# Performance work log

Hardware: AMD Instinct MI355X
Metric: run time of the kernel (lower is better)

Reference implementation:

```python
import jax, jax.numpy as jnp
import numpy as np

TEMP = 0.5
K_SEL = 20
NEG_SLOPE = 0.1


def setup_inputs() -> dict:
    key = jax.random.key(0)
    ks = jax.random.split(key, 12)
    B, N = 64, 20000
    F1, F2, D = 512, 256, 128
    init = lambda k, shape, fan: (jax.random.normal(k, shape) / np.sqrt(fan)).astype(jnp.float32)
    return {
        "patient_embedding": jax.random.normal(ks[0], (B, F1), dtype=jnp.float32),
        "gene_embedding": jax.random.normal(ks[1], (N, F2), dtype=jnp.float32),
        "Wq": init(ks[2], (F1, D), F1), "bq": jnp.zeros((D,), jnp.float32),
        "Wk": init(ks[3], (F2, D), F2), "bk": jnp.zeros((D,), jnp.float32),
        "Wv": init(ks[4], (F2, D), F2), "bv": jnp.zeros((D,), jnp.float32),
        "W1": init(ks[5], (2 * D, D), 2 * D), "b1": jnp.zeros((D,), jnp.float32),
        "w2": init(ks[6], (D,), D), "b2": jnp.zeros((), jnp.float32),
    }


def reference(patient_embedding, gene_embedding, Wq, bq, Wk, bk, Wv, bv, W1, b1, w2, b2):
    B = patient_embedding.shape[0]
    N = gene_embedding.shape[0]
    D = Wq.shape[1]

    Q = patient_embedding @ Wq + bq          # [B, D]
    Km = gene_embedding @ Wk + bk            # [N, D]
    V = gene_embedding @ Wv + bv             # [N, D]

    # MLP attention on cat([Q_exp, K_exp]); split W1 to avoid materializing [B,N,2D]
    q_part = Q @ W1[:D]                      # [B, D]
    k_part = Km @ W1[D:]                     # [N, D]
    h = jax.nn.leaky_relu(q_part[:, None, :] + k_part[None, :, :] + b1, NEG_SLOPE)  # [B, N, D]
    sim = h @ w2 + b2                        # [B, N]
    logits = sim / TEMP

    # gumbel-softmax, hard=True, independent noise per (b, k) row
    g = jax.random.gumbel(jax.random.key(42), (B, K_SEL, N), dtype=logits.dtype)
    y_soft = jax.nn.softmax((logits[:, None, :] + g) / TEMP, axis=-1)   # [B, K, N]
    y_hard = jax.nn.one_hot(jnp.argmax(y_soft, axis=-1), N, dtype=y_soft.dtype)
    masks = y_hard - jax.lax.stop_gradient(y_soft) + y_soft             # straight-through

    topk_values = jnp.einsum("bkn,nd->bkd", masks, V)                   # [B, K, D]
    scores = jnp.einsum("bd,bkd->bk", Q, topk_values) / np.sqrt(D).astype(np.float32)
    weights = jax.nn.softmax(scores, axis=-1)                           # [B, K] (dropout = eval/identity)
    context = jnp.einsum("bk,bkd->bd", weights, topk_values)            # [B, D]
    return context
```

## Files before the change

kernel.cpp:

```cpp
#include <hip/hip_runtime.h>

#define NG 20000

__device__ __forceinline__ unsigned rotl32(unsigned x, int r) {
  return __builtin_amdgcn_alignbit(x, x, 32 - r);
}

__device__ __forceinline__ void threefry2x32(unsigned x0, unsigned x1,
                                             unsigned& o0, unsigned& o1) {
  const unsigned ks0 = 0u;
  const unsigned ks1 = 42u;
  const unsigned ks2 = 0x1BD11BDAu ^ 0u ^ 42u;
  x0 += ks0; x1 += ks1;
#define TFR(r) { x0 += x1; x1 = rotl32(x1, (r)); x1 ^= x0; }
  TFR(13) TFR(15) TFR(26) TFR(6)
  x0 += ks1; x1 += ks2 + 1u;
  TFR(17) TFR(29) TFR(16) TFR(24)
  x0 += ks2; x1 += ks0 + 2u;
  TFR(13) TFR(15) TFR(26) TFR(6)
  x0 += ks0; x1 += ks1 + 3u;
  TFR(17) TFR(29) TFR(16) TFR(24)
  x0 += ks1; x1 += ks2 + 4u;
  TFR(13) TFR(15) TFR(26) TFR(6)
  x0 += ks2; x1 += ks0 + 5u;
#undef TFR
  o0 = x0; o1 = x1;
}

__device__ __forceinline__ unsigned tfbits(unsigned ctr) {
  unsigned o0, o1;
  threefry2x32(0u, ctr, o0, o1);
  return o0 ^ o1;
}

__device__ __forceinline__ float gumbel32(unsigned bits) {
  float f = __uint_as_float((bits >> 9) | 0x3f800000u) - 1.0f;
  float u = fmaxf(f, 1.17549435e-38f);
  const float l2u = __log2f(u);
  return fmaf(-0.69314718056f, __log2f(-l2u), 0.3665129206f);
}

__device__ __forceinline__ double gumbel64(unsigned bits) {
  float f = __uint_as_float((bits >> 9) | 0x3f800000u) - 1.0f;
  double u = (double)fmaxf(f, 1.17549435e-38f);
  return -log(-log(u));
}

__device__ __forceinline__ unsigned long long packcell(double v, int n) {
  unsigned long long u = (unsigned long long)__double_as_longlong(v);
  u = (u >> 63) ? ~u : (u | 0x8000000000000000ull);
  return (u & 0xFFFFFFFFFFFF8000ull) | (unsigned long long)(32767 - n);
}

__device__ __forceinline__ unsigned long long packscreen(float v, int n) {
  unsigned u = __float_as_uint(v);
  u = (u >> 31) ? ~u : (u | 0x80000000u);
  return ((unsigned long long)u << 32) | (unsigned)n;
}

__global__ __launch_bounds__(128) void kprep(
    const float* __restrict__ pe, const float* __restrict__ Wq,
    const float* __restrict__ bq, const float* __restrict__ Wk,
    const float* __restrict__ bk, const float* __restrict__ W1,
    const float* __restrict__ b1, const float* __restrict__ w2,
    float* __restrict__ Wf32, double* __restrict__ qbT,
    float* __restrict__ Qm, unsigned long long* __restrict__ cells,
    double2* __restrict__ c12) {
  __shared__ float L[512];
  __shared__ double Ld[128];
  const int t = threadIdx.x;
  const int bid = blockIdx.x;
  if (bid < 256) {
    L[t] = Wk[bid * 128 + t];
    __syncthreads();
    double acc = 0.0;
    #pragma unroll 16
    for (int j = 0; j < 128; ++j)
      acc = fma((double)L[j], (double)W1[(128 + j) * 128 + t], acc);
    Wf32[bid * 128 + t] = (float)acc;
  } else if (bid < 320) {
    const int b = bid - 256;
    #pragma unroll
    for (int i = 0; i < 4; ++i) L[t + 128 * i] = pe[b * 512 + t + 128 * i];
    __syncthreads();
    double q = (double)bq[t];
    #pragma unroll 16
    for (int f = 0; f < 512; ++f)
      q = fma((double)L[f], (double)Wq[f * 128 + t], q);
    Qm[b * 128 + t] = (float)q;
    Ld[t] = q;
    __syncthreads();
    double acc = (double)b1[t];
    #pragma unroll 8
    for (int j = 0; j < 128; ++j) {
      acc = fma(Ld[j], (double)W1[j * 128 + t], acc);
      acc = fma((double)bk[j], (double)W1[(128 + j) * 128 + t], acc);
    }
    qbT[t * 64 + b] = acc;
  } else {
    for (int i = t; i < 1280; i += 128) cells[i] = 0ull;
    const double w2d = (double)w2[t];
    c12[t] = make_double2(0.55 * w2d, 0.45 * w2d);
  }
}

__global__ __launch_bounds__(256) void ksim(
    const float* __restrict__ ge, const float* __restrict__ Wf32,
    const double* __restrict__ qbT, const double2* __restrict__ c12,
    float* __restrict__ simg) {
  __shared__ double SBd[2048];
  __shared__ float Wt[4096];
  __shared__ float kpL[2048];
  float* geL = (float*)SBd;
  float* simLf = (float*)SBd;
  const int t = threadIdx.x;
  const int wv = t >> 6;
  const int lane = t & 63;
  const int g0 = blockIdx.x * 16;

  {
    const float4* src = (const float4*)(ge + (size_t)g0 * 256);
    float4* dst = (float4*)geL;
    #pragma unroll
    for (int i = 0; i < 4; ++i) dst[t + i * 256] = src[t + i * 256];
  }

  float acc[4][2];
  #pragma unroll
  for (int j = 0; j < 4; ++j) { acc[j][0] = 0.f; acc[j][1] = 0.f; }
  const float* gL = geL + wv * 4 * 256;

  for (int tile = 0; tile < 8; ++tile) {
    __syncthreads();
    {
      const float4* wsrc = (const float4*)(Wf32 + tile * 32 * 128);
      float4* wdst = (float4*)Wt;
      #pragma unroll
      for (int i = 0; i < 4; ++i) wdst[t + i * 256] = wsrc[t + i * 256];
    }
    __syncthreads();
    #pragma unroll
    for (int fr = 0; fr < 32; fr += 4) {
      const int f0 = tile * 32 + fr;
      const float2 w0 = *(const float2*)(Wt + (fr + 0) * 128 + 2 * lane);
      const float2 w1 = *(const float2*)(Wt + (fr + 1) * 128 + 2 * lane);
      const float2 w2 = *(const float2*)(Wt + (fr + 2) * 128 + 2 * lane);
      const float2 w3 = *(const float2*)(Wt + (fr + 3) * 128 + 2 * lane);
      #pragma unroll
      for (int j = 0; j < 4; ++j) {
        const float4 gv = *(const float4*)(gL + j * 256 + f0);
        acc[j][0] = fmaf(gv.x, w0.x, acc[j][0]);
        acc[j][1] = fmaf(gv.x, w0.y, acc[j][1]);
        acc[j][0] = fmaf(gv.y, w1.x, acc[j][0]);
        acc[j][1] = fmaf(gv.y, w1.y, acc[j][1]);
        acc[j][0] = fmaf(gv.z, w2.x, acc[j][0]);
        acc[j][1] = fmaf(gv.z, w2.y, acc[j][1]);
        acc[j][0] = fmaf(gv.w, w3.x, acc[j][0]);
        acc[j][1] = fmaf(gv.w, w3.y, acc[j][1]);
      }
    }
  }

  __syncthreads();
  #pragma unroll
  for (int j = 0; j < 4; ++j)
    ((float2*)(kpL + (wv * 4 + j) * 128))[lane] =
        make_float2(acc[j][0], acc[j][1]);
  __syncthreads();

  double s[4];
  #pragma unroll
  for (int j = 0; j < 4; ++j) s[j] = 0.0;
  for (int dd = 0; dd < 128; ++dd) {
    const double2 cc = c12[dd];
    const double qv = qbT[dd * 64 + lane];
    #pragma unroll
    for (int j = 0; j < 4; ++j) {
      const double kv = (double)kpL[(wv + j * 4) * 128 + dd];
      const double tt = qv + kv;
      s[j] = fma(tt, cc.x, s[j]);
      s[j] = fma(fabs(tt), cc.y, s[j]);
    }
  }
  #pragma unroll
  for (int j = 0; j < 4; ++j)
    simLf[lane * 17 + (wv + j * 4)] = (float)(2.0 * s[j]);
  __syncthreads();

  {
    const int b = t >> 2;
    const int gc = t & 3;
    float4 v;
    v.x = simLf[b * 17 + gc * 4 + 0];
    v.y = simLf[b * 17 + gc * 4 + 1];
    v.z = simLf[b * 17 + gc * 4 + 2];
    v.w = simLf[b * 17 + gc * 4 + 3];
    *(float4*)(simg + (size_t)b * NG + g0 + gc * 4) = v;
  }
}

__global__ __launch_bounds__(256) void kargmax(
    const float* __restrict__ simg, unsigned long long* __restrict__ cells) {
  __shared__ unsigned long long R1s[4], R2s[4];
  const int cell = blockIdx.x >> 1;
  const int wdw = blockIdx.x & 1;
  const int t = threadIdx.x;
  const int wv = t >> 6;
  const int lane = t & 63;
  const int b = (unsigned)cell / 20u;
  const float* sb = simg + (size_t)b * NG;
  const unsigned ib = (unsigned)cell * (unsigned)NG;
  const int base = wdw * 10000;
  const int end = base + 10000;

  float m1 = -3e38f, m2 = -3e38f;
  int n1 = -1, n2 = -1;
  int n = base + t;
  for (; n + 256 < end; n += 512) {
    const unsigned bbA = tfbits(ib + (unsigned)n);
    const unsigned bbB = tfbits(ib + (unsigned)(n + 256));
    const float sA = sb[n] + gumbel32(bbA);
    const float sB = sb[n + 256] + gumbel32(bbB);
    if (sA > m1) { m2 = m1; n2 = n1; m1 = sA; n1 = n; }
    else if (sA > m2) { m2 = sA; n2 = n; }
    if (sB > m1) { m2 = m1; n2 = n1; m1 = sB; n1 = n + 256; }
    else if (sB > m2) { m2 = sB; n2 = n + 256; }
  }
  for (; n < end; n += 256) {
    const unsigned bb = tfbits(ib + (unsigned)n);
    const float sc = sb[n] + gumbel32(bb);
    if (sc > m1) { m2 = m1; n2 = n1; m1 = sc; n1 = n; }
    else if (sc > m2) { m2 = sc; n2 = n; }
  }
  unsigned long long p1 = packscreen(m1, n1);
  unsigned long long p2 = packscreen(m2, n2);
  #pragma unroll
  for (int off = 32; off; off >>= 1) {
    unsigned long long q1 = __shfl_xor(p1, off, 64);
    unsigned long long q2 = __shfl_xor(p2, off, 64);
    if (q1 > p1) {
      unsigned long long t1 = p1;
      p1 = q1;
      p2 = (q2 > t1) ? q2 : t1;
    } else {
      p2 = (q1 > p2) ? q1 : p2;
    }
  }
  if (lane == 0) { R1s[wv] = p1; R2s[wv] = p2; }
  __syncthreads();
  if (t == 0) {
    unsigned long long P1 = R1s[0], P2 = R2s[0];
    #pragma unroll
    for (int w = 1; w < 4; ++w) {
      unsigned long long q1 = R1s[w], q2 = R2s[w];
      if (q1 > P1) {
        unsigned long long t1 = P1;
        P1 = q1;
        P2 = (q2 > t1) ? q2 : t1;
      } else {
        P2 = (q1 > P2) ? q1 : P2;
      }
    }
    const int w1 = (int)(P1 & 0xFFFFFFFFull);
    const int w2i = (int)(P2 & 0xFFFFFFFFull);
    const unsigned bb1 = tfbits(ib + (unsigned)w1);
    const float s1f = sb[w1];
    const float sc1 = s1f + gumbel32(bb1);
    unsigned long long pb = packcell((double)s1f + gumbel64(bb1), w1);
    if (w2i >= 0) {
      const unsigned bb2 = tfbits(ib + (unsigned)w2i);
      const float s2f = sb[w2i];
      const float sc2 = s2f + gumbel32(bb2);
      if ((sc1 - sc2) < 1e-4f) {
        const unsigned long long u2 =
            packcell((double)s2f + gumbel64(bb2), w2i);
        if (u2 > pb) pb = u2;
      }
    }
    atomicMax(&cells[cell], pb);
  }
}

__global__ __launch_bounds__(256) void kfinal(
    const float* __restrict__ ge, const float* __restrict__ Wv,
    const float* __restrict__ bv, const float* __restrict__ Qm,
    const unsigned long long* __restrict__ cells, float* __restrict__ out) {
  const int b = blockIdx.x;
  const int t = threadIdx.x;
  const int wv = t >> 6;
  const int lane = t & 63;
  __shared__ float sc[20];
  __shared__ float ctxp[4][128];
  const float2 qv = ((const float2*)(Qm + b * 128))[lane];
  const float2 bvv = ((const float2*)bv)[lane];
  const float* gr[5];
  float2 V[5];
  #pragma unroll
  for (int j = 0; j < 5; ++j) {
    const unsigned long long cell = cells[b * 20 + wv * 5 + j];
    const int n = 32767 - (int)(cell & 0x7FFFull);
    gr[j] = ge + (size_t)n * 256;
    V[j] = bvv;
  }
  for (int f = 0; f < 256; f += 4) {
    const float2 w0 = ((const float2*)(Wv + (size_t)(f + 0) * 128))[lane];
    const float2 w1 = ((const float2*)(Wv + (size_t)(f + 1) * 128))[lane];
    const float2 w2_ = ((const float2*)(Wv + (size_t)(f + 2) * 128))[lane];
    const float2 w3 = ((const float2*)(Wv + (size_t)(f + 3) * 128))[lane];
    #pragma unroll
    for (int j = 0; j < 5; ++j) {
      const float4 gv = *(const float4*)(gr[j] + f);
      V[j].x = fmaf(gv.x, w0.x, V[j].x); V[j].y = fmaf(gv.x, w0.y, V[j].y);
      V[j].x = fmaf(gv.y, w1.x, V[j].x); V[j].y = fmaf(gv.y, w1.y, V[j].y);
      V[j].x = fmaf(gv.z, w2_.x, V[j].x); V[j].y = fmaf(gv.z, w2_.y, V[j].y);
      V[j].x = fmaf(gv.w, w3.x, V[j].x); V[j].y = fmaf(gv.w, w3.y, V[j].y);
    }
  }
  #pragma unroll
  for (int j = 0; j < 5; ++j) {
    float pr = qv.x * V[j].x + qv.y * V[j].y;
    #pragma unroll
    for (int off = 32; off; off >>= 1) pr += __shfl_xor(pr, off, 64);
    if (lane == 0) sc[wv * 5 + j] = pr * 0.08838834764831845f;
  }
  __syncthreads();
  float m = -3.0e38f;
  #pragma unroll
  for (int i = 0; i < 20; ++i) m = fmaxf(m, sc[i]);
  float s = 0.f;
  #pragma unroll
  for (int i = 0; i < 20; ++i) s += expf(sc[i] - m);
  const float inv = 1.0f / s;
  float c0 = 0.f, c1 = 0.f;
  #pragma unroll
  for (int j = 0; j < 5; ++j) {
    const float wk = expf(sc[wv * 5 + j] - m) * inv;
    c0 = fmaf(wk, V[j].x, c0);
    c1 = fmaf(wk, V[j].y, c1);
  }
  ctxp[wv][2 * lane] = c0;
  ctxp[wv][2 * lane + 1] = c1;
  __syncthreads();
  if (t < 128)
    out[b * 128 + t] = (ctxp[0][t] + ctxp[1][t]) + (ctxp[2][t] + ctxp[3][t]);
}

extern "C" void kernel_launch(void* const* d_in, const int* in_sizes, int n_in,
                              void* d_out, int out_size, void* d_ws, size_t ws_size,
                              hipStream_t stream) {
  (void)in_sizes; (void)n_in; (void)out_size; (void)ws_size;
  const float* pe = (const float*)d_in[0];
  const float* ge = (const float*)d_in[1];
  const float* Wq = (const float*)d_in[2];
  const float* bq = (const float*)d_in[3];
  const float* Wk = (const float*)d_in[4];
  const float* bk = (const float*)d_in[5];
  const float* Wv = (const float*)d_in[6];
  const float* bvp = (const float*)d_in[7];
  const float* W1 = (const float*)d_in[8];
  const float* b1 = (const float*)d_in[9];
  const float* w2 = (const float*)d_in[10];

  char* w = (char*)d_ws;
  float* Wf32 = (float*)w;
  double* qbT = (double*)(w + 131072);
  float* Qm = (float*)(w + 196608);
  unsigned long long* cells =
      (unsigned long long*)(w + 229376);
  double2* c12 = (double2*)(w + 239616);
  float* simg = (float*)(w + 262144);
  float* out = (float*)d_out;

  kprep<<<dim3(321), dim3(128), 0, stream>>>(pe, Wq, bq, Wk, bk, W1, b1, w2,
                                             Wf32, qbT, Qm, cells, c12);
  ksim<<<dim3(1250), dim3(256), 0, stream>>>(ge, Wf32, qbT, c12, simg);
  kargmax<<<dim3(2560), dim3(256), 0, stream>>>(simg, cells);
  kfinal<<<dim3(64), dim3(256), 0, stream>>>(ge, Wv, bvp, Qm, cells, out);
}
```

Baseline: 259.7 us.

## Fuse final context into argmax via last-block counter; widen ksim tiles

The final context kernel is folded into the argmax kernel. A per-batch completion counter, incremented atomically after a threadfence, lets the last of the 40 blocks for a batch row compute the values, scores and context. Separately, the similarity kernel now handles 32 genes per block instead of 16, giving each thread 4x4 register tiles and a paired-dd double loop. Together these remove one kernel launch and improve reuse of the weight tile, at the cost of more registers and shared memory and some tail serialization in the fused finisher.

```diff
diff --git a/kernel.cpp b/kernel.cpp
--- a/kernel.cpp
+++ b/kernel.cpp
@@ -65,7 +65,7 @@
     const float* __restrict__ b1, const float* __restrict__ w2,
     float* __restrict__ Wf32, double* __restrict__ qbT,
     float* __restrict__ Qm, unsigned long long* __restrict__ cells,
-    double2* __restrict__ c12) {
+    double2* __restrict__ c12, int* __restrict__ bdone) {
   __shared__ float L[512];
   __shared__ double Ld[128];
   const int t = threadIdx.x;
@@ -99,6 +99,7 @@
     qbT[t * 64 + b] = acc;
   } else {
     for (int i = t; i < 1280; i += 128) cells[i] = 0ull;
+    if (t < 64) bdone[t] = 0;
     const double w2d = (double)w2[t];
     c12[t] = make_double2(0.55 * w2d, 0.45 * w2d);
   }
@@ -108,27 +109,32 @@
     const float* __restrict__ ge, const float* __restrict__ Wf32,
     const double* __restrict__ qbT, const double2* __restrict__ c12,
     float* __restrict__ simg) {
-  __shared__ double SBd[2048];
-  __shared__ float Wt[4096];
-  __shared__ float kpL[2048];
-  float* geL = (float*)SBd;
-  float* simLf = (float*)SBd;
+  __shared__ float SB[8448];
+  __shared__ float WK[4096];
+  float* geL = SB;
+  float* simLf = SB;
+  float* Wt = WK;
+  float* kpL = WK;
   const int t = threadIdx.x;
   const int wv = t >> 6;
   const int lane = t & 63;
-  const int g0 = blockIdx.x * 16;
+  const int h = lane >> 5;
+  const int sl = lane & 31;
+  const int g0 = blockIdx.x * 32;
 
   {
     const float4* src = (const float4*)(ge + (size_t)g0 * 256);
     float4* dst = (float4*)geL;
     #pragma unroll
-    for (int i = 0; i < 4; ++i) dst[t + i * 256] = src[t + i * 256];
-  }
-
-  float acc[4][2];
-  #pragma unroll
-  for (int j = 0; j < 4; ++j) { acc[j][0] = 0.f; acc[j][1] = 0.f; }
-  const float* gL = geL + wv * 4 * 256;
+    for (int i = 0; i < 8; ++i) dst[t + i * 256] = src[t + i * 256];
+  }
+
+  float acc[4][4];
+  #pragma unroll
+  for (int j = 0; j < 4; ++j)
+    #pragma unroll
+    for (int r = 0; r < 4; ++r) acc[j][r] = 0.f;
+  const float* gL = geL + (wv * 8 + h * 4) * 256;
 
   for (int tile = 0; tile < 8; ++tile) {
     __syncthreads();
@@ -142,21 +148,29 @@
     #pragma unroll
     for (int fr = 0; fr < 32; fr += 4) {
       const int f0 = tile * 32 + fr;
-      const float2 w0 = *(const float2*)(Wt + (fr + 0) * 128 + 2 * lane);
-      const float2 w1 = *(const float2*)(Wt + (fr + 1) * 128 + 2 * lane);
-      const float2 w2 = *(const float2*)(Wt + (fr + 2) * 128 + 2 * lane);
-      const float2 w3 = *(const float2*)(Wt + (fr + 3) * 128 + 2 * lane);
+      const float4 w0 = *(const float4*)(Wt + (fr + 0) * 128 + 4 * sl);
+      const float4 w1 = *(const float4*)(Wt + (fr + 1) * 128 + 4 * sl);
+      const float4 w2 = *(const float4*)(Wt + (fr + 2) * 128 + 4 * sl);
+      const float4 w3 = *(const float4*)(Wt + (fr + 3) * 128 + 4 * sl);
       #pragma unroll
       for (int j = 0; j < 4; ++j) {
         const float4 gv = *(const float4*)(gL + j * 256 + f0);
         acc[j][0] = fmaf(gv.x, w0.x, acc[j][0]);
         acc[j][1] = fmaf(gv.x, w0.y, acc[j][1]);
+        acc[j][2] = fmaf(gv.x, w0.z, acc[j][2]);
+        acc[j][3] = fmaf(gv.x, w0.w, acc[j][3]);
         acc[j][0] = fmaf(gv.y, w1.x, acc[j][0]);
         acc[j][1] = fmaf(gv.y, w1.y, acc[j][1]);
+        acc[j][2] = fmaf(gv.y, w1.z, acc[j][2]);
+        acc[j][3] = fmaf(gv.y, w1.w, acc[j][3]);
         acc[j][0] = fmaf(gv.z, w2.x, acc[j][0]);
         acc[j][1] = fmaf(gv.z, w2.y, acc[j][1]);
+        acc[j][2] = fmaf(gv.z, w2.z, acc[j][2]);
+        acc[j][3] = fmaf(gv.z, w2.w, acc[j][3]);
         acc[j][0] = fmaf(gv.w, w3.x, acc[j][0]);
         acc[j][1] = fmaf(gv.w, w3.y, acc[j][1]);
+        acc[j][2] = fmaf(gv.w, w3.z, acc[j][2]);
+        acc[j][3] = fmaf(gv.w, w3.w, acc[j][3]);
       }
     }
   }
@@ -164,44 +178,57 @@
   __syncthreads();
   #pragma unroll
   for (int j = 0; j < 4; ++j)
-    ((float2*)(kpL + (wv * 4 + j) * 128))[lane] =
-        make_float2(acc[j][0], acc[j][1]);
-  __syncthreads();
-
-  double s[4];
-  #pragma unroll
-  for (int j = 0; j < 4; ++j) s[j] = 0.0;
-  for (int dd = 0; dd < 128; ++dd) {
-    const double2 cc = c12[dd];
-    const double qv = qbT[dd * 64 + lane];
-    #pragma unroll
-    for (int j = 0; j < 4; ++j) {
-      const double kv = (double)kpL[(wv + j * 4) * 128 + dd];
-      const double tt = qv + kv;
-      s[j] = fma(tt, cc.x, s[j]);
-      s[j] = fma(fabs(tt), cc.y, s[j]);
-    }
-  }
-  #pragma unroll
-  for (int j = 0; j < 4; ++j)
-    simLf[lane * 17 + (wv + j * 4)] = (float)(2.0 * s[j]);
-  __syncthreads();
-
-  {
-    const int b = t >> 2;
-    const int gc = t & 3;
+    *(float4*)(kpL + (wv * 8 + h * 4 + j) * 128 + 4 * sl) =
+        make_float4(acc[j][0], acc[j][1], acc[j][2], acc[j][3]);
+  __syncthreads();
+
+  double s[8];
+  #pragma unroll
+  for (int j = 0; j < 8; ++j) s[j] = 0.0;
+  for (int dd = 0; dd < 128; dd += 2) {
+    const double2 cc0 = c12[dd];
+    const double2 cc1 = c12[dd + 1];
+    const double qv0 = qbT[dd * 64 + lane];
+    const double qv1 = qbT[(dd + 1) * 64 + lane];
+    #pragma unroll
+    for (int j = 0; j < 8; ++j) {
+      const float2 kv = *(const float2*)(kpL + (wv * 8 + j) * 128 + dd);
+      const double tt0 = qv0 + (double)kv.x;
+      s[j] = fma(tt0, cc0.x, s[j]);
+      s[j] = fma(fabs(tt0), cc0.y, s[j]);
+      const double tt1 = qv1 + (double)kv.y;
+      s[j] = fma(tt1, cc1.x, s[j]);
+      s[j] = fma(fabs(tt1), cc1.y, s[j]);
+    }
+  }
+  #pragma unroll
+  for (int j = 0; j < 8; ++j)
+    simLf[lane * 33 + (wv * 8 + j)] = (float)(2.0 * s[j]);
+  __syncthreads();
+
+  #pragma unroll
+  for (int p = 0; p < 2; ++p) {
+    const int b = (t >> 3) + 32 * p;
+    const int gc = t & 7;
     float4 v;
-    v.x = simLf[b * 17 + gc * 4 + 0];
-    v.y = simLf[b * 17 + gc * 4 + 1];
-    v.z = simLf[b * 17 + gc * 4 + 2];
-    v.w = simLf[b * 17 + gc * 4 + 3];
+    v.x = simLf[b * 33 + gc * 4 + 0];
+    v.y = simLf[b * 33 + gc * 4 + 1];
+    v.z = simLf[b * 33 + gc * 4 + 2];
+    v.w = simLf[b * 33 + gc * 4 + 3];
     *(float4*)(simg + (size_t)b * NG + g0 + gc * 4) = v;
   }
 }
 
-__global__ __launch_bounds__(256) void kargmax(
-    const float* __restrict__ simg, unsigned long long* __restrict__ cells) {
+__global__ __launch_bounds__(256) void kargfin(
+    const float* __restrict__ simg, const float* __restrict__ ge,
+    const float* __restrict__ Wv, const float* __restrict__ bv,
+    const float* __restrict__ Qm, unsigned long long* __restrict__ cells,
+    int* __restrict__ bdone, float* __restrict__ out) {
   __shared__ unsigned long long R1s[4], R2s[4];
+  __shared__ int fin;
+  __shared__ int nsel[20];
+  __shared__ float sc[20];
+  __shared__ float ctxp[4][128];
   const int cell = blockIdx.x >> 1;
   const int wdw = blockIdx.x & 1;
   const int t = threadIdx.x;
@@ -228,9 +255,9 @@
   }
   for (; n < end; n += 256) {
     const unsigned bb = tfbits(ib + (unsigned)n);
-    const float sc = sb[n] + gumbel32(bb);
-    if (sc > m1) { m2 = m1; n2 = n1; m1 = sc; n1 = n; }
-    else if (sc > m2) { m2 = sc; n2 = n; }
+    const float sc_ = sb[n] + gumbel32(bb);
+    if (sc_ > m1) { m2 = m1; n2 = n1; m1 = sc_; n1 = n; }
+    else if (sc_ > m2) { m2 = sc_; n2 = n; }
   }
   unsigned long long p1 = packscreen(m1, n1);
   unsigned long long p2 = packscreen(m2, n2);
@@ -278,28 +305,23 @@
       }
     }
     atomicMax(&cells[cell], pb);
-  }
-}
-
-__global__ __launch_bounds__(256) void kfinal(
-    const float* __restrict__ ge, const float* __restrict__ Wv,
-    const float* __restrict__ bv, const float* __restrict__ Qm,
-    const unsigned long long* __restrict__ cells, float* __restrict__ out) {
-  const int b = blockIdx.x;
-  const int t = threadIdx.x;
-  const int wv = t >> 6;
-  const int lane = t & 63;
-  __shared__ float sc[20];
-  __shared__ float ctxp[4][128];
+    __threadfence();
+    const int old = atomicAdd(&bdone[b], 1);
+    fin = (old == 39) ? 1 : 0;
+  }
+  __syncthreads();
+  if (!fin) return;
+
+  if (t < 20)
+    nsel[t] = 32767 - (int)(atomicMax(&cells[b * 20 + t], 0ull) & 0x7FFFull);
+  __syncthreads();
   const float2 qv = ((const float2*)(Qm + b * 128))[lane];
   const float2 bvv = ((const float2*)bv)[lane];
   const float* gr[5];
   float2 V[5];
   #pragma unroll
   for (int j = 0; j < 5; ++j) {
-    const unsigned long long cell = cells[b * 20 + wv * 5 + j];
-    const int n = 32767 - (int)(cell & 0x7FFFull);
-    gr[j] = ge + (size_t)n * 256;
+    gr[j] = ge + (size_t)nsel[wv * 5 + j] * 256;
     V[j] = bvv;
   }
   for (int f = 0; f < 256; f += 4) {
@@ -368,12 +390,13 @@
   unsigned long long* cells =
       (unsigned long long*)(w + 229376);
   double2* c12 = (double2*)(w + 239616);
+  int* bdone = (int*)(w + 241664);
   float* simg = (float*)(w + 262144);
   float* out = (float*)d_out;
 
   kprep<<<dim3(321), dim3(128), 0, stream>>>(pe, Wq, bq, Wk, bk, W1, b1, w2,
-                                             Wf32, qbT, Qm, cells, c12);
-  ksim<<<dim3(1250), dim3(256), 0, stream>>>(ge, Wf32, qbT, c12, simg);
-  kargmax<<<dim3(2560), dim3(256), 0, stream>>>(simg, cells);
-  kfinal<<<dim3(64), dim3(256), 0, stream>>>(ge, Wv, bvp, Qm, cells, out);
-}
+                                             Wf32, qbT, Qm, cells, c12, bdone);
+  ksim<<<dim3(625), dim3(256), 0, stream>>>(ge, Wf32, qbT, c12, simg);
+  kargfin<<<dim3(2560), dim3(256), 0, stream>>>(simg, ge, Wv, bvp, Qm, cells,
+                                                bdone, out);
+}
```

New measurement: 317.9 us. 1.22x slower.
